# Kernel tuning notes

Hardware: AMD Instinct MI355X
Metric: run time of the kernel (lower is better)

The kernel has to match this reference:

```python
import jax, jax.numpy as jnp
import numpy as np

B, S, HIDDEN = 1, 2048, 2048
HEADS, HEAD_DIM = 32, 128
EPS = 1e-5
THETA = 10000.0


def setup_inputs() -> dict:
    key = jax.random.key(0)
    k0, k1, k2 = jax.random.split(key, 3)
    hidden_states = jax.random.normal(k0, (B, S, HIDDEN), jnp.float32)
    positions = jnp.broadcast_to(jnp.arange(S, dtype=jnp.int32)[None, :], (B, S))
    qkv_w = jax.random.normal(k1, (3 * HEADS * HEAD_DIM, HIDDEN), jnp.float32) * 0.02
    q_norm_w = jnp.ones((HEAD_DIM,), jnp.float32)
    k_norm_w = jnp.ones((HEAD_DIM,), jnp.float32)
    o_proj_w = jax.random.normal(k2, (HIDDEN, HEADS * HEAD_DIM), jnp.float32) * 0.02
    return {"hidden_states": hidden_states, "positions": positions, "qkv_w": qkv_w,
            "q_norm_w": q_norm_w, "k_norm_w": k_norm_w, "o_proj_w": o_proj_w}


def _rmsnorm(x, w):
    # RMSNorm over last (head_dim) axis
    var = jnp.mean(x * x, axis=-1, keepdims=True)
    return x * jax.lax.rsqrt(var + EPS) * w


def _rope(x, positions):
    # NeoX-style (non-interleaved) rotary over full head_dim
    d2 = HEAD_DIM // 2
    inv_freq = 1.0 / (THETA ** (jnp.arange(0, HEAD_DIM, 2, dtype=jnp.float32) / HEAD_DIM))
    freqs = positions.astype(jnp.float32)[..., None] * inv_freq  # [B,S,d2]
    cos = jnp.cos(freqs)[:, :, None, :]  # [B,S,1,d2]
    sin = jnp.sin(freqs)[:, :, None, :]
    x1, x2 = x[..., :d2], x[..., d2:]
    return jnp.concatenate([x1 * cos - x2 * sin, x2 * cos + x1 * sin], axis=-1)


def reference(hidden_states, positions, qkv_w, q_norm_w, k_norm_w, o_proj_w):
    b, s, _ = hidden_states.shape
    qkv = jnp.einsum('bsh,oh->bso', hidden_states, qkv_w)  # [B,S,3*H*D]
    q, k, v = jnp.split(qkv, 3, axis=-1)
    q = q.reshape(b, s, HEADS, HEAD_DIM)
    k = k.reshape(b, s, HEADS, HEAD_DIM)
    v = v.reshape(b, s, HEADS, HEAD_DIM)
    # qk_norm (per-head RMSNorm)
    q = _rmsnorm(q, q_norm_w)
    k = _rmsnorm(k, k_norm_w)
    # rotary embedding
    q = _rope(q, positions)
    k = _rope(k, positions)
    # causal attention, scale = head_dim**-0.5 (flash_attn default)
    scale = HEAD_DIM ** -0.5
    scores = jnp.einsum('bqhd,bkhd->bhqk', q, k) * scale  # [B,H,S,S]
    causal = jnp.tril(jnp.ones((s, s), dtype=bool))
    scores = jnp.where(causal[None, None], scores, jnp.float32(-1e30))
    probs = jax.nn.softmax(scores, axis=-1)
    o = jnp.einsum('bhqk,bkhd->bqhd', probs, v).reshape(b, s, HEADS * HEAD_DIM)
    return jnp.einsum('bso,ho->bsh', o, o_proj_w)
```

## Files before the change

### kernel.cpp

```cpp
#include <hip/hip_runtime.h>
#include <cstdint>
#include <cstddef>

static constexpr int S_LEN = 2048;
static constexpr int HID   = 2048;
static constexpr int NH    = 32;
static constexpr int HD    = 128;
static constexpr int OD    = 4096;
static constexpr int QKV_O = 12288;

#define AS1 __attribute__((address_space(1)))
#define AS3 __attribute__((address_space(3)))

typedef __attribute__((ext_vector_type(8))) short bf16x8;
typedef __attribute__((ext_vector_type(4))) float f32x4;
typedef __attribute__((ext_vector_type(4))) short s16x4;

template <int V> struct IC { static constexpr int v = V; };

__device__ __forceinline__ short f2bf(float f) {
  unsigned u = __float_as_uint(f);
  unsigned r = (u + 0x7fffu + ((u >> 16) & 1u)) >> 16;
  return (short)r;
}
__device__ __forceinline__ float bf2f(short s) {
  return __uint_as_float(((unsigned)(unsigned short)s) << 16);
}
__device__ __forceinline__ unsigned pk2bf(float a, float b) {
  return __builtin_amdgcn_perm(__float_as_uint(b), __float_as_uint(a), 0x07060302u);
}

__global__ void convert2_kernel(const float* __restrict__ in1, short* __restrict__ out1, int n1_4,
                                const float* __restrict__ in2, short* __restrict__ out2, int n2_4) {
  int i = blockIdx.x * blockDim.x + threadIdx.x;
  const float* in; short* out; int j;
  if (i < n1_4) { in = in1; out = out1; j = i; }
  else { j = i - n1_4; if (j >= n2_4) return; in = in2; out = out2; }
  float4 f = ((const float4*)in)[i == j ? i : j];
  s16x4 s;
  s.x = f2bf(f.x); s.y = f2bf(f.y); s.z = f2bf(f.z); s.w = f2bf(f.w);
  ((s16x4*)out)[j] = s;
}

template <int BNT, int CMODE>
__global__ __launch_bounds__(512, 2) void gemm8p(
    const short* __restrict__ A, const short* __restrict__ Bw, void* __restrict__ Cp,
    int K, int N, int ldc) {
  constexpr int BH  = BNT / 128;
  constexpr int NJ  = BNT / 64;
  constexpr int NJH = NJ / 2;
  __shared__ short Al[2][128 * 64];
  __shared__ short Bl[2][BH][128 * 64];
  const int tid  = threadIdx.x;
  const int lane = tid & 63;
  const int quad = lane >> 4;
  const int col  = lane & 15;
  const int wave = tid >> 6;
  const int wm   = wave >> 2;
  const int wn   = wave & 3;

  const int cpx = gridDim.x >> 3;
  const int bid = blockIdx.x;
  const int swz = (bid & 7) * cpx + (bid >> 3);
  const int nbn = N / BNT;
  const int m0  = (swz / nbn) * 128;
  const int n0  = (swz % nbn) * BNT;

  const int NT = K >> 6;

  f32x4 acc[4][NJ] = {};
  bf16x8 a[4][2], b0[NJH][2], b1[NJH][2];

  auto stA = [&](int t, int buf) {
#pragma unroll
    for (int r = 0; r < 2; ++r) {
      int idx = r * 512 + tid;
      int row = idx >> 3;
      int g   = idx & 7;
      int gs  = g ^ ((row >> 1) & 7);
      const short* ga = A + (size_t)(m0 + row) * K + t * 64 + gs * 8;
      __builtin_amdgcn_global_load_lds((const AS1 unsigned*)ga,
                                       (AS3 unsigned*)&Al[buf][idx * 8], 16, 0, 0);
    }
  };
  auto stB = [&](int t, int buf, int h) {
#pragma unroll
    for (int r = 0; r < 2; ++r) {
      int idx = r * 512 + tid;
      int row = idx >> 3;
      int g   = idx & 7;
      int gs  = g ^ ((row >> 1) & 7);
      const short* gb = Bw + (size_t)(n0 + h * 128 + row) * K + t * 64 + gs * 8;
      __builtin_amdgcn_global_load_lds((const AS1 unsigned*)gb,
                                       (AS3 unsigned*)&Bl[buf][h][idx * 8], 16, 0, 0);
    }
  };
  auto rdA = [&](int buf, int mh) {
#pragma unroll
    for (int i = 0; i < 2; ++i) {
      int rh = wm * 64 + (mh * 2 + i) * 16 + col;
#pragma unroll
      for (int kf = 0; kf < 2; ++kf)
        a[mh * 2 + i][kf] =
            *(const bf16x8*)&Al[buf][rh * 64 + (((kf * 4 + quad) ^ ((rh >> 1) & 7)) * 8)];
    }
  };
  auto rdB = [&](int buf, int nh, bf16x8 (&bb)[NJH][2]) {
#pragma unroll
    for (int j = 0; j < NJH; ++j) {
      int br = wn * (BNT / 4) + nh * (BNT / 8) + j * 16 + col;
      int bh = br >> 7, rh = br & 127;
#pragma unroll
      for (int kf = 0; kf < 2; ++kf)
        bb[j][kf] =
            *(const bf16x8*)&Bl[buf][bh][rh * 64 + (((kf * 4 + quad) ^ ((rh >> 1) & 7)) * 8)];
    }
  };
  auto mm = [&](auto MH, auto NHc, bf16x8 (&bb)[NJH][2]) {
    constexpr int mh = MH.v, nh = NHc.v;
    __builtin_amdgcn_s_setprio(1);
#pragma unroll
    for (int i = 0; i < 2; ++i)
#pragma unroll
      for (int j = 0; j < NJH; ++j)
#pragma unroll
        for (int kf = 0; kf < 2; ++kf)
          acc[mh * 2 + i][nh * NJH + j] = __builtin_amdgcn_mfma_f32_16x16x32_bf16(
              a[mh * 2 + i][kf], bb[j][kf], acc[mh * 2 + i][nh * NJH + j], 0, 0, 0);
    __builtin_amdgcn_s_setprio(0);
  };
#define LGK() do { asm volatile("s_waitcnt lgkmcnt(0)"); __builtin_amdgcn_sched_barrier(0); } while (0)
#define BAR() __builtin_amdgcn_s_barrier()
  auto vmc_mid = [] {
    if constexpr (BH == 3) asm volatile("s_waitcnt vmcnt(6)" ::: "memory");
    else                   asm volatile("s_waitcnt vmcnt(4)" ::: "memory");
  };
  auto vmc_end = [] {
    if constexpr (BH == 3) asm volatile("s_waitcnt vmcnt(8)" ::: "memory");
    else                   asm volatile("s_waitcnt vmcnt(4)" ::: "memory");
  };

#pragma unroll
  for (int h = 0; h < BH; ++h) stB(0, 0, h);
  stA(0, 0);
#pragma unroll
  for (int h = 0; h < BH; ++h) stB(1, 1, h);
  stA(1, 1);
  if constexpr (BH == 3) asm volatile("s_waitcnt vmcnt(8)" ::: "memory");
  else                   asm volatile("s_waitcnt vmcnt(4)" ::: "memory");
  BAR();

  for (int i = 0; i < (NT >> 1); ++i) {
    const int t  = 2 * i;
    const int tA = (t + 2 < NT) ? t + 2 : NT - 2;
    const int tB = (t + 3 < NT) ? t + 3 : NT - 1;
    rdA(0, 0); rdB(0, 0, b0);
    BAR(); LGK();
    mm(IC<0>{}, IC<0>{}, b0);
    BAR();
    rdB(0, 1, b1);
    BAR(); LGK();
    mm(IC<0>{}, IC<1>{}, b1);
    BAR();
    rdA(0, 1);
    stB(tA, 0, 0);
    BAR(); LGK();
    mm(IC<1>{}, IC<1>{}, b1);
    BAR();
    if constexpr (BH == 3) stB(tA, 0, 1);
    stA(tA, 0);
    BAR();
    mm(IC<1>{}, IC<0>{}, b0);
    vmc_mid();
    BAR();
    rdA(1, 0); rdB(1, 0, b0);
    if constexpr (BH == 3) stB(tA, 0, 2);
    BAR(); LGK();
    mm(IC<0>{}, IC<0>{}, b0);
    BAR();
    rdB(1, 1, b1);
    BAR(); LGK();
    mm(IC<0>{}, IC<1>{}, b1);
    BAR();
    rdA(1, 1);
    stB(tB, 1, 0);
    if constexpr (BH == 3) stB(tB, 1, 1);
    BAR(); LGK();
    mm(IC<1>{}, IC<1>{}, b1);
    BAR();
    if constexpr (BH == 3) stB(tB, 1, 2);
    stA(tB, 1);
    BAR();
    mm(IC<1>{}, IC<0>{}, b0);
    vmc_end();
    BAR();
  }
#undef LGK
#undef BAR

#pragma unroll
  for (int mi = 0; mi < 4; ++mi)
#pragma unroll
    for (int nj = 0; nj < NJ; ++nj)
#pragma unroll
      for (int r = 0; r < 4; ++r) {
        int rr = m0 + wm * 64 + mi * 16 + quad * 4 + r;
        int cc = n0 + wn * (BNT / 4) + nj * 16 + col;
        if (CMODE == 1)
          ((float*)Cp)[(size_t)rr * ldc + cc] = acc[mi][nj][r];
        else
          ((short*)Cp)[(size_t)rr * ldc + cc] = f2bf(acc[mi][nj][r]);
      }
}

#define BM 128
#define BK 32

template <int BNT, int CMODE>
__global__ __launch_bounds__(256, 2) void gemm_nt_f32w(
    const short* __restrict__ A, const float* __restrict__ B, void* __restrict__ Cp,
    int K, int ldc) {
  __shared__ short Alds[2][BM * BK];
  __shared__ short Blds[2][BNT * BK];
  constexpr int WN  = BNT / 2;
  constexpr int NJ  = WN / 16;
  constexpr int BCH = (BNT * 4) / 256;
  const int tid  = threadIdx.x;
  const int lane = tid & 63;
  const int quad = lane >> 4;
  const int col  = lane & 15;
  const int wave = tid >> 6;
  const int m0 = blockIdx.y * BM;
  const int n0 = blockIdx.x * BNT;
  const int wm = (wave & 1) * 64;
  const int wn = (wave >> 1) * WN;

  f32x4 acc[4][NJ] = {};
  float4 breg[BCH][2];

  const int nk = K / BK;

  auto b_issue = [&](int k0) {
#pragma unroll
    for (int it = 0; it < BCH; ++it) {
      int idx = it * 256 + tid;
      int row = idx >> 2;
      int c   = idx & 3;
      const float* gb = B + (size_t)(n0 + row) * K + k0 + c * 8;
      breg[it][0] = *(const float4*)gb;
      breg[it][1] = *(const float4*)(gb + 4);
    }
  };
  auto a_issue = [&](int k0, int buf) {
#pragma unroll
    for (int it = 0; it < 2; ++it) {
      int idx = it * 256 + tid;
      int row = idx >> 2;
      int c   = idx & 3;
      int cs  = c ^ ((row >> 1) & 3);
      const short* ga = A + (size_t)(m0 + row) * K + k0 + cs * 8;
      __builtin_amdgcn_global_load_lds((const AS1 unsigned*)ga,
                                       (AS3 unsigned*)&Alds[buf][idx * 8], 16, 0, 0);
    }
  };
  auto b_write = [&](int buf) {
#pragma unroll
    for (int it = 0; it < BCH; ++it) {
      int idx = it * 256 + tid;
      int row = idx >> 2;
      int c   = idx & 3;
      int cw  = c ^ ((row >> 1) & 3);
      union { unsigned u[4]; bf16x8 v; } pk;
      pk.u[0] = pk2bf(breg[it][0].x, breg[it][0].y);
      pk.u[1] = pk2bf(breg[it][0].z, breg[it][0].w);
      pk.u[2] = pk2bf(breg[it][1].x, breg[it][1].y);
      pk.u[3] = pk2bf(breg[it][1].z, breg[it][1].w);
      *(bf16x8*)&Blds[buf][(row * 4 + cw) * 8] = pk.v;
    }
  };
  auto compute = [&](int buf) {
    bf16x8 a[4], b[NJ];
#pragma unroll
    for (int i = 0; i < 4; ++i) {
      int row = wm + i * 16 + col;
      a[i] = *(const bf16x8*)&Alds[buf][(row * 4 + (quad ^ ((row >> 1) & 3))) * 8];
    }
#pragma unroll
    for (int j = 0; j < NJ; ++j) {
      int row = wn + j * 16 + col;
      b[j] = *(const bf16x8*)&Blds[buf][(row * 4 + (quad ^ ((row >> 1) & 3))) * 8];
    }
#pragma unroll
    for (int i = 0; i < 4; ++i)
#pragma unroll
      for (int j = 0; j < NJ; ++j)
        acc[i][j] = __builtin_amdgcn_mfma_f32_16x16x32_bf16(a[i], b[j], acc[i][j], 0, 0, 0);
  };

  b_issue(0);
  a_issue(0, 0);
  b_write(0);
  __syncthreads();

  for (int t = 0; t < nk - 1; ++t) {
    const int cur = t & 1;
    b_issue((t + 1) * BK);
    a_issue((t + 1) * BK, cur ^ 1);
    compute(cur);
    b_write(cur ^ 1);
    __syncthreads();
  }
  compute((nk - 1) & 1);

#pragma unroll
  for (int i = 0; i < 4; ++i)
#pragma unroll
    for (int j = 0; j < NJ; ++j)
#pragma unroll
      for (int r = 0; r < 4; ++r) {
        int rr = m0 + wm + i * 16 + quad * 4 + r;
        int cc = n0 + wn + j * 16 + col;
        if (CMODE == 1)
          ((float*)Cp)[(size_t)rr * ldc + cc] = acc[i][j][r];
        else
          ((short*)Cp)[(size_t)rr * ldc + cc] = f2bf(acc[i][j][r]);
      }
}

__global__ void normrope_packv_kernel(short* __restrict__ qkv,
                                      const int* __restrict__ positions,
                                      const float* __restrict__ qw,
                                      const float* __restrict__ kw,
                                      short* __restrict__ vtp) {
  __shared__ short T[64][136];
  if (blockIdx.x < 32768) {
    int item = blockIdx.x * 4 + (threadIdx.x >> 6);
    int lane = threadIdx.x & 63;
    int head  = item & 31;
    int which = (item >> 5) & 1;
    int s     = item >> 6;
    const float* w = which ? kw : qw;
    short* base = qkv + (size_t)s * QKV_O + which * OD + head * HD;

    float x1 = bf2f(base[lane]);
    float x2 = bf2f(base[lane + 64]);
    float ss = x1 * x1 + x2 * x2;
#pragma unroll
    for (int d = 32; d; d >>= 1) ss += __shfl_xor(ss, d);
    float r = rsqrtf(ss * (1.0f / 128.0f) + 1e-5f);
    float xn1 = x1 * r * w[lane];
    float xn2 = x2 * r * w[lane + 64];

    float pos = (float)positions[s];
    float inv_freq = exp2f((float)lane * (-13.287712379549449f / 64.0f));
    float f = pos * inv_freq;
    float c = cosf(f), sn = sinf(f);
    float sc = which ? 1.0f : 0.12751863738f;
    base[lane]      = f2bf((xn1 * c - xn2 * sn) * sc);
    base[lane + 64] = f2bf((xn2 * c + xn1 * sn) * sc);
  } else {
    int bid2 = blockIdx.x - 32768;
    const int h  = bid2 & 31;
    const int kt = bid2 >> 5;
    const int tid = threadIdx.x;
    {
      int rr = tid >> 2;
      int db = (tid & 3) * 32;
      const short* src = qkv + (size_t)(kt * 64 + rr) * QKV_O + 2 * OD + h * HD + db;
#pragma unroll
      for (int i = 0; i < 4; ++i)
        *(bf16x8*)&T[rr][db + i * 8] = *(const bf16x8*)(src + i * 8);
    }
    __syncthreads();
    {
      int d  = tid >> 1;
      int k0 = (tid & 1) * 32;
      short* dst = vtp + (((size_t)h * 32 + kt) * 128 + d) * 64 + k0;
#pragma unroll
      for (int c = 0; c < 4; ++c) {
        bf16x8 v;
#pragma unroll
        for (int j = 0; j < 8; ++j) v[j] = T[k0 + c * 8 + j][d];
        *(bf16x8*)&dst[c * 8] = v;
      }
    }
  }
}

__global__ __launch_bounds__(256, 2) void attn_kernel(
    const short* __restrict__ qkv, const short* __restrict__ vtp, short* __restrict__ obuf) {
  __shared__ short Klds[2][64 * 128];
  __shared__ short Vt[2][128 * 64];
  __shared__ short Plds[4][16 * 64];

  const int tid  = threadIdx.x;
  const int lane = tid & 63;
  const int wave = tid >> 6;
  const int quad = lane >> 4;
  const int col  = lane & 15;
  const int h    = blockIdx.y;

  const int kr  = tid >> 2;
  const int kcb = (tid & 3) * 32;
  const int vd  = tid >> 1;
  const int vcb = (tid & 1) * 32;

  bf16x8 kreg[4], vreg[4];

  auto loadK = [&](int kt) {
    const short* kp = qkv + (size_t)(kt * 64 + kr) * QKV_O + OD + h * HD + kcb;
#pragma unroll
    for (int i = 0; i < 4; ++i) kreg[i] = *(const bf16x8*)(kp + i * 8);
  };
  auto loadV = [&](int kt) {
    const short* vp = vtp + (((size_t)h * 32 + kt) * 128 + vd) * 64 + vcb;
#pragma unroll
    for (int i = 0; i < 4; ++i) vreg[i] = *(const bf16x8*)(vp + i * 8);
  };
  auto writeKV = [&](int buf) {
#pragma unroll
    for (int i = 0; i < 4; ++i) {
      int swz = ((tid & 3) * 4 + i) ^ (kr & 15);
      *(bf16x8*)&Klds[buf][kr * 128 + swz * 8] = kreg[i];
    }
#pragma unroll
    for (int i = 0; i < 4; ++i) {
      int swz = ((tid & 1) * 4 + i) ^ (vd & 7);
      *(bf16x8*)&Vt[buf][vd * 64 + swz * 8] = vreg[i];
    }
  };

#pragma unroll 1
  for (int half = 0; half < 2; ++half) {
    const int qt = half == 0 ? blockIdx.x : 31 - blockIdx.x;
    const int qbase = qt * 64 + wave * 16;

    bf16x8 qf[4];
#pragma unroll
    for (int kf = 0; kf < 4; ++kf)
      qf[kf] = *(const bf16x8*)(qkv + (size_t)(qbase + col) * QKV_O + h * HD + kf * 32 + quad * 8);

    f32x4 o[8] = {};
    float m_r[4], l_i[4];
#pragma unroll
    for (int r = 0; r < 4; ++r) { m_r[r] = -1e30f; l_i[r] = 0.f; }

    loadK(0); loadV(0);
    __syncthreads();
    writeKV(0);

#pragma unroll 1
    for (int kt = 0; kt <= qt; ++kt) {
      const int cur = kt & 1;
      if (kt < qt) { loadK(kt + 1); loadV(kt + 1); }
      __syncthreads();

      f32x4 sfr[4];
#pragma unroll
      for (int nf = 0; nf < 4; ++nf) {
        f32x4 acc = {};
#pragma unroll
        for (int kf = 0; kf < 4; ++kf) {
          bf16x8 b = *(const bf16x8*)&Klds[cur][(nf * 16 + col) * 128 + ((kf * 4 + quad) ^ col) * 8];
          acc = __builtin_amdgcn_mfma_f32_16x16x32_bf16(qf[kf], b, acc, 0, 0, 0);
        }
        sfr[nf] = acc;
      }

      if (kt == qt) {
#pragma unroll
        for (int nf = 0; nf < 4; ++nf)
#pragma unroll
          for (int r = 0; r < 4; ++r) {
            int key = kt * 64 + nf * 16 + col;
            int qg  = qbase + quad * 4 + r;
            if (key > qg) sfr[nf][r] = -1e30f;
          }
      }

#pragma unroll
      for (int r = 0; r < 4; ++r) {
        float mt = fmaxf(fmaxf(sfr[0][r], sfr[1][r]), fmaxf(sfr[2][r], sfr[3][r]));
#pragma unroll
        for (int d = 8; d; d >>= 1) mt = fmaxf(mt, __shfl_xor(mt, d));
        float mnew  = fmaxf(m_r[r], mt);
        float alpha = exp2f(m_r[r] - mnew);
        float ps = 0.f;
#pragma unroll
        for (int nf = 0; nf < 4; ++nf) {
          float p = exp2f(sfr[nf][r] - mnew);
          sfr[nf][r] = p;
          ps += p;
        }
        l_i[r] = l_i[r] * alpha + ps;
        m_r[r] = mnew;
#pragma unroll
        for (int nf = 0; nf < 8; ++nf) o[nf][r] *= alpha;
      }

#pragma unroll
      for (int nf = 0; nf < 4; ++nf)
#pragma unroll
        for (int r = 0; r < 4; ++r) {
          int row = quad * 4 + r;
          int key = nf * 16 + col;
          Plds[wave][row * 64 + ((key >> 3) ^ (row & 7)) * 8 + (key & 7)] = f2bf(sfr[nf][r]);
        }

      bf16x8 pa[2];
#pragma unroll
      for (int kf = 0; kf < 2; ++kf)
        pa[kf] = *(const bf16x8*)&Plds[wave][col * 64 + ((kf * 4 + quad) ^ (col & 7)) * 8];
#pragma unroll
      for (int nf = 0; nf < 8; ++nf)
#pragma unroll
        for (int kf = 0; kf < 2; ++kf) {
          bf16x8 vb = *(const bf16x8*)&Vt[cur][(nf * 16 + col) * 64 + ((kf * 4 + quad) ^ (col & 7)) * 8];
          o[nf] = __builtin_amdgcn_mfma_f32_16x16x32_bf16(pa[kf], vb, o[nf], 0, 0, 0);
        }

      if (kt < qt) writeKV(cur ^ 1);
    }

#pragma unroll
    for (int r = 0; r < 4; ++r) {
      float lt = l_i[r];
#pragma unroll
      for (int d = 8; d; d >>= 1) lt += __shfl_xor(lt, d);
      float inv = 1.0f / lt;
      int sg = qbase + quad * 4 + r;
#pragma unroll
      for (int nf = 0; nf < 8; ++nf)
        obuf[(size_t)sg * OD + h * HD + nf * 16 + col] = f2bf(o[nf][r] * inv);
    }
  }
}

extern "C" void kernel_launch(void* const* d_in, const int* in_sizes, int n_in,
                              void* d_out, int out_size, void* d_ws, size_t ws_size,
                              hipStream_t stream) {
  (void)in_sizes; (void)n_in; (void)out_size;
  const float* hs   = (const float*)d_in[0];
  const int*   pos  = (const int*)d_in[1];
  const float* qkvw = (const float*)d_in[2];
  const float* qw   = (const float*)d_in[3];
  const float* kw   = (const float*)d_in[4];
  const float* ow   = (const float*)d_in[5];
  float* out = (float*)d_out;

  char* ws = (char*)d_ws;
  short* qkvb    = (short*)(ws);
  short* obuf    = (short*)(ws + 50331648);
  short* qkvw_bf = (short*)(ws + 67108864);
  short* ow_bf   = (short*)(ws + 67108864);
  short* hsb  = (short*)d_out;
  short* vtp  = (short*)d_out;

  const bool fast = ws_size >= (size_t)117440512;

  if (fast) {
    int n1 = (S_LEN * HID) / 4, n2 = (QKV_O * HID) / 4;
    convert2_kernel<<<(n1 + n2 + 255) / 256, 256, 0, stream>>>(hs, hsb, n1, qkvw, qkvw_bf, n2);
    gemm8p<384, 0><<<(S_LEN / 128) * (QKV_O / 384), 512, 0, stream>>>(
        hsb, qkvw_bf, qkvb, HID, QKV_O, QKV_O);
    int n3 = (HID * OD) / 4;
    convert2_kernel<<<(n3 + 255) / 256, 256, 0, stream>>>(ow, ow_bf, n3, ow, ow_bf, 0);
  } else {
    int n1 = (S_LEN * HID) / 4;
    convert2_kernel<<<(n1 + 255) / 256, 256, 0, stream>>>(hs, hsb, n1, hs, hsb, 0);
    gemm_nt_f32w<128, 0><<<dim3(QKV_O / 128, S_LEN / BM), 256, 0, stream>>>(
        hsb, qkvw, qkvb, HID, QKV_O);
  }

  normrope_packv_kernel<<<(S_LEN * 2 * NH) / 4 + NH * (S_LEN / 64), 256, 0, stream>>>(
      qkvb, pos, qw, kw, vtp);

  attn_kernel<<<dim3(16, NH), 256, 0, stream>>>(qkvb, vtp, obuf);

  if (fast) {
    gemm8p<128, 1><<<(S_LEN / 128) * (HID / 128), 512, 0, stream>>>(
        obuf, ow_bf, out, OD, HID, HID);
  } else {
    gemm_nt_f32w<64, 1><<<dim3(HID / 64, S_LEN / BM), 256, 0, stream>>>(
        obuf, ow, out, OD, HID);
  }
}
```

Before: 494.7 us.

## Retile QKV GEMM, remap blocks per XCD, single-buffer attention LDS with lazy rescale

The QKV projection GEMM switches from 384-wide to 256-wide N tiles, with vmcnt waits added for the two-B-half case. Block-to-tile mapping in the GEMM now assigns contiguous N column ranges to each XCD for L2 locality. The attention kernel drops K/V LDS double buffering so it can target 3 blocks per CU, raises wave priority around the MFMA sections, and skips the output rescale when the running max grows by at most 8 (in log2 units) across the wave. Single buffering adds an extra barrier per tile, and the deferred rescale risks larger exponent ranges, though it is bounded.

Result: no change. 490.7 us (-0.8%).

```diff
diff --git a/kernel.cpp b/kernel.cpp
--- a/kernel.cpp
+++ b/kernel.cpp
@@ -36,7 +36,7 @@
   const float* in; short* out; int j;
   if (i < n1_4) { in = in1; out = out1; j = i; }
   else { j = i - n1_4; if (j >= n2_4) return; in = in2; out = out2; }
-  float4 f = ((const float4*)in)[i == j ? i : j];
+  float4 f = ((const float4*)in)[j];
   s16x4 s;
   s.x = f2bf(f.x); s.y = f2bf(f.y); s.z = f2bf(f.z); s.w = f2bf(f.w);
   ((s16x4*)out)[j] = s;
@@ -59,12 +59,12 @@
   const int wm   = wave >> 2;
   const int wn   = wave & 3;
 
-  const int cpx = gridDim.x >> 3;
-  const int bid = blockIdx.x;
-  const int swz = (bid & 7) * cpx + (bid >> 3);
   const int nbn = N / BNT;
-  const int m0  = (swz / nbn) * 128;
-  const int n0  = (swz % nbn) * BNT;
+  const int nbm = gridDim.x / nbn;
+  const int xcd = blockIdx.x & 7;
+  const int u   = blockIdx.x >> 3;
+  const int m0  = (u % nbm) * 128;
+  const int n0  = (xcd * (nbn >> 3) + u / nbm) * BNT;
 
   const int NT = K >> 6;
 
@@ -132,12 +132,13 @@
 #define LGK() do { asm volatile("s_waitcnt lgkmcnt(0)"); __builtin_amdgcn_sched_barrier(0); } while (0)
 #define BAR() __builtin_amdgcn_s_barrier()
   auto vmc_mid = [] {
-    if constexpr (BH == 3) asm volatile("s_waitcnt vmcnt(6)" ::: "memory");
-    else                   asm volatile("s_waitcnt vmcnt(4)" ::: "memory");
+    if constexpr (BH == 1) asm volatile("s_waitcnt vmcnt(4)" ::: "memory");
+    else                   asm volatile("s_waitcnt vmcnt(6)" ::: "memory");
   };
   auto vmc_end = [] {
-    if constexpr (BH == 3) asm volatile("s_waitcnt vmcnt(8)" ::: "memory");
-    else                   asm volatile("s_waitcnt vmcnt(4)" ::: "memory");
+    if constexpr (BH == 1)      asm volatile("s_waitcnt vmcnt(4)" ::: "memory");
+    else if constexpr (BH == 2) asm volatile("s_waitcnt vmcnt(6)" ::: "memory");
+    else                        asm volatile("s_waitcnt vmcnt(8)" ::: "memory");
   };
 
 #pragma unroll
@@ -146,8 +147,9 @@
 #pragma unroll
   for (int h = 0; h < BH; ++h) stB(1, 1, h);
   stA(1, 1);
-  if constexpr (BH == 3) asm volatile("s_waitcnt vmcnt(8)" ::: "memory");
-  else                   asm volatile("s_waitcnt vmcnt(4)" ::: "memory");
+  if constexpr (BH == 1)      asm volatile("s_waitcnt vmcnt(4)" ::: "memory");
+  else if constexpr (BH == 2) asm volatile("s_waitcnt vmcnt(6)" ::: "memory");
+  else                        asm volatile("s_waitcnt vmcnt(8)" ::: "memory");
   BAR();
 
   for (int i = 0; i < (NT >> 1); ++i) {
@@ -167,7 +169,7 @@
     BAR(); LGK();
     mm(IC<1>{}, IC<1>{}, b1);
     BAR();
-    if constexpr (BH == 3) stB(tA, 0, 1);
+    if constexpr (BH >= 2) stB(tA, 0, 1);
     stA(tA, 0);
     BAR();
     mm(IC<1>{}, IC<0>{}, b0);
@@ -184,7 +186,7 @@
     BAR();
     rdA(1, 1);
     stB(tB, 1, 0);
-    if constexpr (BH == 3) stB(tB, 1, 1);
+    if constexpr (BH >= 2) stB(tB, 1, 1);
     BAR(); LGK();
     mm(IC<1>{}, IC<1>{}, b1);
     BAR();
@@ -387,10 +389,10 @@
   }
 }
 
-__global__ __launch_bounds__(256, 2) void attn_kernel(
+__global__ __launch_bounds__(256, 3) void attn_kernel(
     const short* __restrict__ qkv, const short* __restrict__ vtp, short* __restrict__ obuf) {
-  __shared__ short Klds[2][64 * 128];
-  __shared__ short Vt[2][128 * 64];
+  __shared__ short Klds[64 * 128];
+  __shared__ short Vt[128 * 64];
   __shared__ short Plds[4][16 * 64];
 
   const int tid  = threadIdx.x;
@@ -417,16 +419,16 @@
 #pragma unroll
     for (int i = 0; i < 4; ++i) vreg[i] = *(const bf16x8*)(vp + i * 8);
   };
-  auto writeKV = [&](int buf) {
+  auto writeKV = [&]() {
 #pragma unroll
     for (int i = 0; i < 4; ++i) {
       int swz = ((tid & 3) * 4 + i) ^ (kr & 15);
-      *(bf16x8*)&Klds[buf][kr * 128 + swz * 8] = kreg[i];
+      *(bf16x8*)&Klds[kr * 128 + swz * 8] = kreg[i];
     }
 #pragma unroll
     for (int i = 0; i < 4; ++i) {
       int swz = ((tid & 1) * 4 + i) ^ (vd & 7);
-      *(bf16x8*)&Vt[buf][vd * 64 + swz * 8] = vreg[i];
+      *(bf16x8*)&Vt[vd * 64 + swz * 8] = vreg[i];
     }
   };
 
@@ -446,26 +448,27 @@
     for (int r = 0; r < 4; ++r) { m_r[r] = -1e30f; l_i[r] = 0.f; }
 
     loadK(0); loadV(0);
-    __syncthreads();
-    writeKV(0);
 
 #pragma unroll 1
     for (int kt = 0; kt <= qt; ++kt) {
-      const int cur = kt & 1;
+      __syncthreads();
+      writeKV();
+      __syncthreads();
       if (kt < qt) { loadK(kt + 1); loadV(kt + 1); }
-      __syncthreads();
 
       f32x4 sfr[4];
+      __builtin_amdgcn_s_setprio(1);
 #pragma unroll
       for (int nf = 0; nf < 4; ++nf) {
         f32x4 acc = {};
 #pragma unroll
         for (int kf = 0; kf < 4; ++kf) {
-          bf16x8 b = *(const bf16x8*)&Klds[cur][(nf * 16 + col) * 128 + ((kf * 4 + quad) ^ col) * 8];
+          bf16x8 b = *(const bf16x8*)&Klds[(nf * 16 + col) * 128 + ((kf * 4 + quad) ^ col) * 8];
           acc = __builtin_amdgcn_mfma_f32_16x16x32_bf16(qf[kf], b, acc, 0, 0, 0);
         }
         sfr[nf] = acc;
       }
+      __builtin_amdgcn_s_setprio(0);
 
       if (kt == qt) {
 #pragma unroll
@@ -483,7 +486,9 @@
         float mt = fmaxf(fmaxf(sfr[0][r], sfr[1][r]), fmaxf(sfr[2][r], sfr[3][r]));
 #pragma unroll
         for (int d = 8; d; d >>= 1) mt = fmaxf(mt, __shfl_xor(mt, d));
-        float mnew  = fmaxf(m_r[r], mt);
+        float mnew = fmaxf(m_r[r], mt);
+        bool defer = __all(mnew - m_r[r] <= 8.0f);
+        if (defer) mnew = m_r[r];
         float alpha = exp2f(m_r[r] - mnew);
         float ps = 0.f;
 #pragma unroll
@@ -493,9 +498,11 @@
           ps += p;
         }
         l_i[r] = l_i[r] * alpha + ps;
-        m_r[r] = mnew;
-#pragma unroll
-        for (int nf = 0; nf < 8; ++nf) o[nf][r] *= alpha;
+        if (!defer) {
+#pragma unroll
+          for (int nf = 0; nf < 8; ++nf) o[nf][r] *= alpha;
+          m_r[r] = mnew;
+        }
       }
 
 #pragma unroll
@@ -511,15 +518,15 @@
 #pragma unroll
       for (int kf = 0; kf < 2; ++kf)
         pa[kf] = *(const bf16x8*)&Plds[wave][col * 64 + ((kf * 4 + quad) ^ (col & 7)) * 8];
+      __builtin_amdgcn_s_setprio(1);
 #pragma unroll
       for (int nf = 0; nf < 8; ++nf)
 #pragma unroll
         for (int kf = 0; kf < 2; ++kf) {
-          bf16x8 vb = *(const bf16x8*)&Vt[cur][(nf * 16 + col) * 64 + ((kf * 4 + quad) ^ (col & 7)) * 8];
+          bf16x8 vb = *(const bf16x8*)&Vt[(nf * 16 + col) * 64 + ((kf * 4 + quad) ^ (col & 7)) * 8];
           o[nf] = __builtin_amdgcn_mfma_f32_16x16x32_bf16(pa[kf], vb, o[nf], 0, 0, 0);
         }
-
-      if (kt < qt) writeKV(cur ^ 1);
+      __builtin_amdgcn_s_setprio(0);
     }
 
 #pragma unroll
@@ -561,7 +568,7 @@
   if (fast) {
     int n1 = (S_LEN * HID) / 4, n2 = (QKV_O * HID) / 4;
     convert2_kernel<<<(n1 + n2 + 255) / 256, 256, 0, stream>>>(hs, hsb, n1, qkvw, qkvw_bf, n2);
-    gemm8p<384, 0><<<(S_LEN / 128) * (QKV_O / 384), 512, 0, stream>>>(
+    gemm8p<256, 0><<<(S_LEN / 128) * (QKV_O / 256), 512, 0, stream>>>(
         hsb, qkvw_bf, qkvb, HID, QKV_O, QKV_O);
     int n3 = (HID * OD) / 4;
     convert2_kernel<<<(n3 + 255) / 256, 256, 0, stream>>>(ow, ow_bf, n3, ow, ow_bf, 0);
```
